# Optimization experiments

Hardware: AMD Instinct MI355X
Metric: run time of the kernel (lower is better)

## Reference

```python
import jax, jax.numpy as jnp
import numpy as np

B, S, HID = 4, 2048, 1024
NH, NKV, HD = 16, 4, 64
GROUPS = NH // NKV
SCALE = HD ** -0.5


def make_rope(seq_len, dim, base=10000.0):
    inv_freq = 1.0 / (base ** (np.arange(0, dim, 2, dtype=np.float32) / dim))
    t = np.arange(seq_len, dtype=np.float32)
    freqs = np.outer(t, inv_freq)                      # [S, D/2]
    emb = np.concatenate([freqs, freqs], axis=-1)      # [S, D] duplicated-half convention
    cos = jnp.asarray(np.cos(emb))[None, None]         # [1,1,S,D]
    sin = jnp.asarray(np.sin(emb))[None, None]
    return cos, sin


def setup_inputs() -> dict:
    key = jax.random.key(0)
    ks = jax.random.split(key, 8)
    hidden_states = jax.random.normal(ks[0], (B, S, HID), dtype=jnp.float32)
    cos, sin = make_rope(S, HD)
    std = HID ** -0.5
    Wq = jax.random.normal(ks[1], (NH * HD, HID), dtype=jnp.float32) * std
    bq = jnp.zeros((NH * HD,), dtype=jnp.float32)
    Wk = jax.random.normal(ks[2], (NKV * HD, HID), dtype=jnp.float32) * std
    bk = jnp.zeros((NKV * HD,), dtype=jnp.float32)
    Wv = jax.random.normal(ks[3], (NKV * HD, HID), dtype=jnp.float32) * std
    bv = jnp.zeros((NKV * HD,), dtype=jnp.float32)
    Wo = jax.random.normal(ks[4], (HID, NH * HD), dtype=jnp.float32) * std
    bo = jnp.zeros((HID,), dtype=jnp.float32)
    return dict(hidden_states=hidden_states, cos=cos, sin=sin,
                Wq=Wq, bq=bq, Wk=Wk, bk=bk, Wv=Wv, bv=bv, Wo=Wo, bo=bo)


def rotate_half(x):
    x1, x2 = jnp.split(x, 2, axis=-1)
    return jnp.concatenate([-x2, x1], axis=-1)


def reference(hidden_states, cos, sin, Wq, bq, Wk, bk, Wv, bv, Wo, bo):
    x = hidden_states  # [B,S,HID]
    q = (x @ Wq.T + bq).reshape(B, S, NH, HD).transpose(0, 2, 1, 3)    # [B,NH,S,D]
    k = (x @ Wk.T + bk).reshape(B, S, NKV, HD).transpose(0, 2, 1, 3)   # [B,NKV,S,D]
    v = (x @ Wv.T + bv).reshape(B, S, NKV, HD).transpose(0, 2, 1, 3)
    # RoPE
    q = q * cos + rotate_half(q) * sin
    k = k * cos + rotate_half(k) * sin
    # GQA: repeat_interleave kv heads to match q heads
    k = jnp.repeat(k, GROUPS, axis=1)  # [B,NH,S,D]
    v = jnp.repeat(v, GROUPS, axis=1)
    # scaled dot-product attention (no mask, no dropout at eval)
    scores = jnp.einsum('bhqd,bhkd->bhqk', q, k) * SCALE
    attn = jax.nn.softmax(scores, axis=-1)
    out = jnp.einsum('bhqk,bhkd->bhqd', attn, v)       # [B,NH,S,D]
    out = out.transpose(0, 2, 1, 3).reshape(B, S, NH * HD)
    return out @ Wo.T + bo
```

## Files before the change

### kernel.cpp

```cpp
#include <hip/hip_runtime.h>
#include <stdint.h>

#define S_LEN 2048
#define HIDDEN 1024
#define NHEADS 16
#define NKVH 4
#define HDIM 64

typedef __bf16 bf16x8 __attribute__((ext_vector_type(8)));
typedef __bf16 bf16x4 __attribute__((ext_vector_type(4)));
typedef float f32x4 __attribute__((ext_vector_type(4)));
typedef short s16x4 __attribute__((ext_vector_type(4)));
typedef unsigned short U16;

#define OFF_XB   0u
#define OFF_WQB  8388608u
#define OFF_WKB  9437184u
#define OFF_WVB  9699328u
#define OFF_WOB  9961472u
#define OFF_Q    11010048u
#define OFF_K    19398656u
#define OFF_V    21495808u
#define OFF_AWS  OFF_XB

static __device__ __forceinline__ U16 f2bf(float f){
    unsigned u;
    __builtin_memcpy(&u, &f, 4);
    u += 0x7FFFu + ((u >> 16) & 1u);
    return (U16)(u >> 16);
}
static __device__ __forceinline__ uint32_t pkbf(float lo, float hi){
    uint32_t a, b;
    __builtin_memcpy(&a, &lo, 4); a += 0x7FFFu + ((a >> 16) & 1u);
    __builtin_memcpy(&b, &hi, 4); b += 0x7FFFu + ((b >> 16) & 1u);
    return (a >> 16) | (b & 0xFFFF0000u);
}

typedef __attribute__((address_space(3))) uint32_t lds_u32;
typedef const __attribute__((address_space(1))) uint32_t glb_u32;
static __device__ __forceinline__ void glds16(const U16* g, U16* l){
    __builtin_amdgcn_global_load_lds((glb_u32*)g, (lds_u32*)l, 16, 0, 0);
}

__global__ void conv_kernel(const float* __restrict__ X,  const float* __restrict__ Wq,
                            const float* __restrict__ Wk, const float* __restrict__ Wv,
                            const float* __restrict__ Wo, U16* __restrict__ dst)
{
    size_t i4 = (size_t)blockIdx.x * 256 + threadIdx.x;
    size_t e = i4 * 4;
    const float* s;
    if (e < 8388608u)       s = X  + e;
    else if (e < 9437184u)  s = Wq + (e - 8388608u);
    else if (e < 9699328u)  s = Wk + (e - 9437184u);
    else if (e < 9961472u)  s = Wv + (e - 9699328u);
    else                    s = Wo + (e - 9961472u);
    float4 v = *(const float4*)s;
    uint2 o; o.x = pkbf(v.x, v.y); o.y = pkbf(v.z, v.w);
    *(uint2*)(dst + e) = o;
}

__global__ __launch_bounds__(256, 3)
void qkv_kernel(const U16* __restrict__ Xb,
                const U16* __restrict__ Wqb, const U16* __restrict__ Wkb, const U16* __restrict__ Wvb,
                const float* __restrict__ bq, const float* __restrict__ bk, const float* __restrict__ bv,
                const float* __restrict__ cosT, const float* __restrict__ sinT,
                U16* __restrict__ qws, U16* __restrict__ kws, U16* __restrict__ vtws)
{
    __shared__ __align__(16) U16 Asm[128 * 64];
    __shared__ __align__(16) U16 Bsm[128 * 64];

    const int mblk = blockIdx.x;
    const int nblk = blockIdx.y;
    const int tid  = threadIdx.x;
    const int wave = tid >> 6, lane = tid & 63;
    const int ln = lane & 15, quad = lane >> 4;
    const int wm = wave >> 1, wn = wave & 1;

    const U16* Wp; const float* biasp; int region;
    const int nbase = nblk * 128;
    if (nblk < 8)       { Wp = Wqb + (size_t)nbase * HIDDEN;          biasp = bq + nbase;          region = 0; }
    else if (nblk < 10) { Wp = Wkb + (size_t)(nbase - 1024) * HIDDEN; biasp = bk + (nbase - 1024); region = 1; }
    else                { Wp = Wvb + (size_t)(nbase - 1280) * HIDDEN; biasp = bv + (nbase - 1280); region = 2; }
    const U16* Xp = Xb + (size_t)mblk * 128 * HIDDEN;

    f32x4 acc[4][4];
    #pragma unroll
    for (int i = 0; i < 4; i++)
        #pragma unroll
        for (int j = 0; j < 4; j++) acc[i][j] = (f32x4){0.f, 0.f, 0.f, 0.f};

    const int l8 = lane >> 3;
    const int cg = (lane & 7) ^ l8;
    const int sw = ln & 7;

    for (int k0 = 0; k0 < HIDDEN; k0 += 64) {
        __syncthreads();
        #pragma unroll
        for (int t = 0; t < 4; t++) {
            int rbase = wave * 32 + t * 8;
            glds16(Xp + (size_t)(rbase + l8) * HIDDEN + k0 + cg * 8, &Asm[rbase * 64]);
            glds16(Wp + (size_t)(rbase + l8) * HIDDEN + k0 + cg * 8, &Bsm[rbase * 64]);
        }
        __syncthreads();

        bf16x8 af[4][2], bfr[4][2];
        #pragma unroll
        for (int i = 0; i < 4; i++)
            #pragma unroll
            for (int ks = 0; ks < 2; ks++) {
                af[i][ks]  = *(const bf16x8*)(&Asm[(wm * 64 + i * 16 + ln) * 64 + (((ks * 4 + quad) ^ sw) * 8)]);
                bfr[i][ks] = *(const bf16x8*)(&Bsm[(wn * 64 + i * 16 + ln) * 64 + (((ks * 4 + quad) ^ sw) * 8)]);
            }
        #pragma unroll
        for (int i = 0; i < 4; i++)
            #pragma unroll
            for (int j = 0; j < 4; j++) {
                acc[i][j] = __builtin_amdgcn_mfma_f32_16x16x32_bf16(af[i][0], bfr[j][0], acc[i][j], 0, 0, 0);
                acc[i][j] = __builtin_amdgcn_mfma_f32_16x16x32_bf16(af[i][1], bfr[j][1], acc[i][j], 0, 0, 0);
            }
    }

    float bias[4];
    #pragma unroll
    for (int j = 0; j < 4; j++) bias[j] = biasp[wn * 64 + j * 16 + ln];

    const float QSCALE = 0.125f * 1.44269504089f;

    if (region == 2) {
        #pragma unroll
        for (int i = 0; i < 4; i++) {
            int m0 = mblk * 128 + wm * 64 + i * 16 + quad * 4;
            int b = m0 >> 11;
            int st6 = m0 & (S_LEN - 1);
            int tile = st6 >> 6, soff = st6 & 63;
            #pragma unroll
            for (int j = 0; j < 4; j++) {
                int n2 = nbase - 1280 + wn * 64 + j * 16 + ln;
                int hh = n2 >> 6, d = n2 & 63;
                uint2 w;
                w.x = pkbf(acc[i][j][0] + bias[j], acc[i][j][1] + bias[j]);
                w.y = pkbf(acc[i][j][2] + bias[j], acc[i][j][3] + bias[j]);
                *(uint2*)(vtws + ((((size_t)b * NKVH + hh) * 32 + tile) * 64 + d) * 64 + soff) = w;
            }
        }
    } else {
        #pragma unroll
        for (int i = 0; i < 4; i++) {
            #pragma unroll
            for (int r = 0; r < 4; r++) {
                int m = mblk * 128 + wm * 64 + i * 16 + quad * 4 + r;
                int s = m & (S_LEN - 1), b = m >> 11;
                float vals[4];
                #pragma unroll
                for (int j = 0; j < 4; j++) vals[j] = acc[i][j][r] + bias[j];
                float outv[4];
                #pragma unroll
                for (int j = 0; j < 4; j++) {
                    int d = (wn * 64 + j * 16 + ln) & 63;
                    float c  = cosT[s * HDIM + d];
                    float sn = sinT[s * HDIM + d];
                    float partner = vals[j ^ 2];
                    float rot = (d < 32) ? -partner : partner;
                    outv[j] = vals[j] * c + rot * sn;
                }
                if (region == 0) {
                    #pragma unroll
                    for (int j = 0; j < 4; j++) {
                        int n = nbase + wn * 64 + j * 16 + ln;
                        int hh = n >> 6, d = n & 63;
                        qws[(((size_t)b * NHEADS + hh) * S_LEN + s) * HDIM + d] = f2bf(outv[j] * QSCALE);
                    }
                } else {
                    #pragma unroll
                    for (int j = 0; j < 4; j++) {
                        int n2 = nbase - 1024 + wn * 64 + j * 16 + ln;
                        int hh = n2 >> 6, d = n2 & 63;
                        kws[(((size_t)b * NKVH + hh) * S_LEN + s) * HDIM + d] = f2bf(outv[j]);
                    }
                }
            }
        }
    }
}

__global__ __launch_bounds__(256, 4)
void attn_kernel(const U16* __restrict__ qws, const U16* __restrict__ kws,
                 const U16* __restrict__ vtws, U16* __restrict__ aws)
{
    __shared__ __align__(16) U16 Ksm[2][64 * 64];
    __shared__ __align__(16) U16 VTsm[2][64 * 64];

    const int qt = blockIdx.x;
    const int hg = blockIdx.y;
    const int b = hg >> 4, h = hg & 15, hkv = h >> 2;
    const U16* Qh  = qws  + (size_t)hg * S_LEN * HDIM;
    const U16* Kh  = kws  + (size_t)(b * NKVH + hkv) * S_LEN * HDIM;
    const U16* VTh = vtws + (size_t)(b * NKVH + hkv) * HDIM * S_LEN;

    const int tid = threadIdx.x;
    const int wave = tid >> 6, lane = tid & 63;
    const int ln = lane & 15, quad = lane >> 4;
    const int sw = ln & 7;
    const int voff = (quad & 1) * 4;

    bf16x8 qf[2][2];
    #pragma unroll
    for (int i = 0; i < 2; i++)
        #pragma unroll
        for (int ks = 0; ks < 2; ks++) {
            int row = qt * 128 + wave * 32 + i * 16 + ln;
            qf[i][ks] = *(const bf16x8*)(Qh + (size_t)row * HDIM + ks * 32 + quad * 8);
        }

    float rsA[2] = {0.f, 0.f}, rsB[2] = {0.f, 0.f};
    f32x4 o_t[4][2];
    #pragma unroll
    for (int n = 0; n < 4; n++)
        #pragma unroll
        for (int i = 0; i < 2; i++) o_t[n][i] = (f32x4){0.f, 0.f, 0.f, 0.f};

    const int l8 = lane >> 3;
    const int cgk = (lane & 7) ^ l8;

    const int koff0 = ln * 64 + ((quad ^ sw) * 8);
    const int koff1 = ln * 64 + (((quad + 4) ^ sw) * 8);
    const int vbase = ln * 64 + voff;
    int cvo[4];
    #pragma unroll
    for (int j = 0; j < 4; j++) cvo[j] = (((j * 2 + (quad >> 1)) ^ sw) * 8);

    const U16* pk[2]; const U16* pv[2];
    U16* dK[2]; U16* dV[2];
    #pragma unroll
    for (int t = 0; t < 2; t++) {
        int c = wave * 2 + t;
        pk[t] = Kh  + (size_t)(c * 8 + l8) * HDIM + cgk * 8;
        pv[t] = VTh + (size_t)(c * 8 + l8) * 64  + cgk * 8;
        dK[t] = &Ksm[0][c * 8 * 64];
        dV[t] = &VTsm[0][c * 8 * 64];
    }

    #pragma unroll
    for (int t = 0; t < 2; t++) {
        glds16(pk[t], dK[t]);
        glds16(pv[t], dV[t]);
        pk[t] += 4096; pv[t] += 4096;
    }

    s16x4 pfp[2];
    pfp[0] = (s16x4){0, 0, 0, 0}; pfp[1] = (s16x4){0, 0, 0, 0};
    s16x4 vfp[4];
    #pragma unroll
    for (int n = 0; n < 4; n++) vfp[n] = (s16x4){0, 0, 0, 0};

    int p = 0;
    for (int kt = 0; kt < 32; kt++) {
        __syncthreads();

        if (kt < 31) {
            #pragma unroll
            for (int t = 0; t < 2; t++) {
                glds16(pk[t], dK[t] + (p ^ 1) * 4096);
                glds16(pv[t], dV[t] + (p ^ 1) * 4096);
                pk[t] += 4096; pv[t] += 4096;
            }
        }

        const U16* Kb = &Ksm[p][0];
        const U16* Vb = &VTsm[p][0];

        bf16x8 kfa = *(const bf16x8*)(Kb + koff0);
        bf16x8 kfb = *(const bf16x8*)(Kb + koff1);

        #pragma unroll
        for (int j = 0; j < 4; j++) {
            __builtin_amdgcn_s_setprio(1);
            f32x4 z[2];
            #pragma unroll
            for (int i = 0; i < 2; i++) {
                z[i] = (f32x4){0.f, 0.f, 0.f, 0.f};
                z[i] = __builtin_amdgcn_mfma_f32_16x16x32_bf16(kfa, qf[i][0], z[i], 0, 0, 0);
                z[i] = __builtin_amdgcn_mfma_f32_16x16x32_bf16(kfb, qf[i][1], z[i], 0, 0, 0);
            }
            #pragma unroll
            for (int n = 0; n < 4; n++)
                #pragma unroll
                for (int i = 0; i < 2; i++)
                    o_t[n][i] = __builtin_amdgcn_mfma_f32_16x16x16bf16_1k(vfp[n], pfp[i], o_t[n][i], 0, 0, 0);
            __builtin_amdgcn_s_setprio(0);

            if (j < 3) {
                kfa = *(const bf16x8*)(Kb + (j + 1) * 1024 + koff0);
                kfb = *(const bf16x8*)(Kb + (j + 1) * 1024 + koff1);
            }
            s16x4 vf[4];
            const U16* Vj = Vb + vbase + cvo[j];
            #pragma unroll
            for (int n = 0; n < 4; n++)
                vf[n] = *(const s16x4*)(Vj + n * 1024);
            __builtin_amdgcn_sched_barrier(0);

            s16x4 pf[2];
            #pragma unroll
            for (int i = 0; i < 2; i++) {
                bf16x4 pb;
                #pragma unroll
                for (int r = 0; r < 4; r++) {
                    float pe = __builtin_amdgcn_exp2f(z[i][r]);
                    if (r & 1) rsB[i] += pe; else rsA[i] += pe;
                    pb[r] = (__bf16)pe;
                }
                __builtin_memcpy(&pf[i], &pb, 8);
            }
            #pragma unroll
            for (int n = 0; n < 4; n++) vfp[n] = vf[n];
            pfp[0] = pf[0]; pfp[1] = pf[1];
        }
        p ^= 1;
    }

    #pragma unroll
    for (int n = 0; n < 4; n++)
        #pragma unroll
        for (int i = 0; i < 2; i++)
            o_t[n][i] = __builtin_amdgcn_mfma_f32_16x16x16bf16_1k(vfp[n], pfp[i], o_t[n][i], 0, 0, 0);

    float inv_li[2];
    #pragma unroll
    for (int i = 0; i < 2; i++) {
        float t = rsA[i] + rsB[i];
        t += __shfl_xor(t, 16);
        t += __shfl_xor(t, 32);
        inv_li[i] = 1.f / t;
    }
    #pragma unroll
    for (int n = 0; n < 4; n++)
        #pragma unroll
        for (int i = 0; i < 2; i++) {
            int q = qt * 128 + wave * 32 + i * 16 + ln;
            int d = n * 16 + quad * 4;
            uint2 w;
            w.x = pkbf(o_t[n][i][0] * inv_li[i], o_t[n][i][1] * inv_li[i]);
            w.y = pkbf(o_t[n][i][2] * inv_li[i], o_t[n][i][3] * inv_li[i]);
            *(uint2*)(aws + ((size_t)b * S_LEN + q) * (NHEADS * HDIM) + h * HDIM + d) = w;
        }
}

__global__ __launch_bounds__(256, 3)
void proj_kernel(const U16* __restrict__ A, const U16* __restrict__ Wob,
                 const float* __restrict__ bo, float* __restrict__ out)
{
    __shared__ __align__(16) U16 Asm[128 * 64];
    __shared__ __align__(16) U16 Bsm[128 * 64];

    const int mblk = blockIdx.x;
    const int nblk = blockIdx.y;
    const int tid  = threadIdx.x;
    const int wave = tid >> 6, lane = tid & 63;
    const int ln = lane & 15, quad = lane >> 4;
    const int wm = wave >> 1, wn = wave & 1;

    const int nbase = nblk * 128;
    const U16* Wp = Wob + (size_t)nbase * HIDDEN;
    const U16* Ap = A + (size_t)mblk * 128 * HIDDEN;

    f32x4 acc[4][4];
    #pragma unroll
    for (int i = 0; i < 4; i++)
        #pragma unroll
        for (int j = 0; j < 4; j++) acc[i][j] = (f32x4){0.f, 0.f, 0.f, 0.f};

    const int l8 = lane >> 3;
    const int cg = (lane & 7) ^ l8;
    const int sw = ln & 7;

    for (int k0 = 0; k0 < HIDDEN; k0 += 64) {
        __syncthreads();
        #pragma unroll
        for (int t = 0; t < 4; t++) {
            int rbase = wave * 32 + t * 8;
            glds16(Ap + (size_t)(rbase + l8) * HIDDEN + k0 + cg * 8, &Asm[rbase * 64]);
            glds16(Wp + (size_t)(rbase + l8) * HIDDEN + k0 + cg * 8, &Bsm[rbase * 64]);
        }
        __syncthreads();

        bf16x8 af[4][2], bfr[4][2];
        #pragma unroll
        for (int i = 0; i < 4; i++)
            #pragma unroll
            for (int ks = 0; ks < 2; ks++) {
                af[i][ks]  = *(const bf16x8*)(&Asm[(wm * 64 + i * 16 + ln) * 64 + (((ks * 4 + quad) ^ sw) * 8)]);
                bfr[i][ks] = *(const bf16x8*)(&Bsm[(wn * 64 + i * 16 + ln) * 64 + (((ks * 4 + quad) ^ sw) * 8)]);
            }
        #pragma unroll
        for (int i = 0; i < 4; i++)
            #pragma unroll
            for (int j = 0; j < 4; j++) {
                acc[i][j] = __builtin_amdgcn_mfma_f32_16x16x32_bf16(af[i][0], bfr[j][0], acc[i][j], 0, 0, 0);
                acc[i][j] = __builtin_amdgcn_mfma_f32_16x16x32_bf16(af[i][1], bfr[j][1], acc[i][j], 0, 0, 0);
            }
    }

    float bias[4];
    #pragma unroll
    for (int j = 0; j < 4; j++) bias[j] = bo[nbase + wn * 64 + j * 16 + ln];

    #pragma unroll
    for (int i = 0; i < 4; i++)
        #pragma unroll
        for (int r = 0; r < 4; r++) {
            int m = mblk * 128 + wm * 64 + i * 16 + quad * 4 + r;
            #pragma unroll
            for (int j = 0; j < 4; j++) {
                int n = nbase + wn * 64 + j * 16 + ln;
                out[(size_t)m * HIDDEN + n] = acc[i][j][r] + bias[j];
            }
        }
}

extern "C" void kernel_launch(void* const* d_in, const int* in_sizes, int n_in,
                              void* d_out, int out_size, void* d_ws, size_t ws_size,
                              hipStream_t stream)
{
    const float* X    = (const float*)d_in[0];
    const float* cosT = (const float*)d_in[1];
    const float* sinT = (const float*)d_in[2];
    const float* Wq   = (const float*)d_in[3];
    const float* bq   = (const float*)d_in[4];
    const float* Wk   = (const float*)d_in[5];
    const float* bk   = (const float*)d_in[6];
    const float* Wv   = (const float*)d_in[7];
    const float* bv   = (const float*)d_in[8];
    const float* Wo   = (const float*)d_in[9];
    const float* bo   = (const float*)d_in[10];
    float* out = (float*)d_out;

    U16* wsb = (U16*)d_ws;
    U16* Xb   = wsb + OFF_XB;
    U16* Wqb  = wsb + OFF_WQB;
    U16* Wkb  = wsb + OFF_WKB;
    U16* Wvb  = wsb + OFF_WVB;
    U16* Wob  = wsb + OFF_WOB;
    U16* qws  = wsb + OFF_Q;
    U16* kws  = wsb + OFF_K;
    U16* vtws = wsb + OFF_V;
    U16* aws  = wsb + OFF_AWS;

    conv_kernel<<<dim3(10752), 256, 0, stream>>>(X, Wq, Wk, Wv, Wo, wsb);
    qkv_kernel<<<dim3(64, 12), 256, 0, stream>>>(Xb, Wqb, Wkb, Wvb, bq, bk, bv, cosT, sinT, qws, kws, vtws);
    attn_kernel<<<dim3(16, 64), 256, 0, stream>>>(qws, kws, vtws, aws);
    proj_kernel<<<dim3(64, 8), 256, 0, stream>>>(aws, Wob, bo, out);
}
```

Before: 244.7 us.

## Use K=32 MFMA for PV product with permuted V-transpose layout

The PV product now uses 16x16x32 bf16 MFMAs in place of 16x16x16. Two 16-key score tiles are processed per step, so each P fragment packs eight probabilities. The projection kernel writes V-transposed with a permuted sequence offset so that each lane's 8-element V fragment lines up with the P element ordering. This halves the PV MFMA count and the number of LDS V reads, but raises register pressure from the doubled score and K fragments.

```diff
diff --git a/kernel.cpp b/kernel.cpp
--- a/kernel.cpp
+++ b/kernel.cpp
@@ -133,6 +133,7 @@
             int b = m0 >> 11;
             int st6 = m0 & (S_LEN - 1);
             int tile = st6 >> 6, soff = st6 & 63;
+            int sperm = (soff & 32) + (((soff & 15) >> 2) << 3) + (((soff >> 4) & 1) << 2);
             #pragma unroll
             for (int j = 0; j < 4; j++) {
                 int n2 = nbase - 1280 + wn * 64 + j * 16 + ln;
@@ -140,7 +141,7 @@
                 uint2 w;
                 w.x = pkbf(acc[i][j][0] + bias[j], acc[i][j][1] + bias[j]);
                 w.y = pkbf(acc[i][j][2] + bias[j], acc[i][j][3] + bias[j]);
-                *(uint2*)(vtws + ((((size_t)b * NKVH + hh) * 32 + tile) * 64 + d) * 64 + soff) = w;
+                *(uint2*)(vtws + ((((size_t)b * NKVH + hh) * 32 + tile) * 64 + d) * 64 + sperm) = w;
             }
         }
     } else {
@@ -201,7 +202,6 @@
     const int wave = tid >> 6, lane = tid & 63;
     const int ln = lane & 15, quad = lane >> 4;
     const int sw = ln & 7;
-    const int voff = (quad & 1) * 4;
 
     bf16x8 qf[2][2];
     #pragma unroll
@@ -224,10 +224,7 @@
 
     const int koff0 = ln * 64 + ((quad ^ sw) * 8);
     const int koff1 = ln * 64 + (((quad + 4) ^ sw) * 8);
-    const int vbase = ln * 64 + voff;
-    int cvo[4];
-    #pragma unroll
-    for (int j = 0; j < 4; j++) cvo[j] = (((j * 2 + (quad >> 1)) ^ sw) * 8);
+    const int vrow = ln * 64;
 
     const U16* pk[2]; const U16* pv[2];
     U16* dK[2]; U16* dV[2];
@@ -247,11 +244,12 @@
         pk[t] += 4096; pv[t] += 4096;
     }
 
-    s16x4 pfp[2];
-    pfp[0] = (s16x4){0, 0, 0, 0}; pfp[1] = (s16x4){0, 0, 0, 0};
-    s16x4 vfp[4];
-    #pragma unroll
-    for (int n = 0; n < 4; n++) vfp[n] = (s16x4){0, 0, 0, 0};
+    bf16x8 pfp[2];
+    #pragma unroll
+    for (int i = 0; i < 2; i++) pfp[i] = (bf16x8){0,0,0,0,0,0,0,0};
+    bf16x8 vfp[4];
+    #pragma unroll
+    for (int n = 0; n < 4; n++) vfp[n] = (bf16x8){0,0,0,0,0,0,0,0};
 
     int p = 0;
     for (int kt = 0; kt < 32; kt++) {
@@ -269,48 +267,56 @@
         const U16* Kb = &Ksm[p][0];
         const U16* Vb = &VTsm[p][0];
 
-        bf16x8 kfa = *(const bf16x8*)(Kb + koff0);
-        bf16x8 kfb = *(const bf16x8*)(Kb + koff1);
-
-        #pragma unroll
-        for (int j = 0; j < 4; j++) {
+        bf16x8 kf[2][2];
+        kf[0][0] = *(const bf16x8*)(Kb + koff0);
+        kf[0][1] = *(const bf16x8*)(Kb + koff1);
+        kf[1][0] = *(const bf16x8*)(Kb + 1024 + koff0);
+        kf[1][1] = *(const bf16x8*)(Kb + 1024 + koff1);
+
+        #pragma unroll
+        for (int pr = 0; pr < 2; pr++) {
             __builtin_amdgcn_s_setprio(1);
-            f32x4 z[2];
-            #pragma unroll
-            for (int i = 0; i < 2; i++) {
-                z[i] = (f32x4){0.f, 0.f, 0.f, 0.f};
-                z[i] = __builtin_amdgcn_mfma_f32_16x16x32_bf16(kfa, qf[i][0], z[i], 0, 0, 0);
-                z[i] = __builtin_amdgcn_mfma_f32_16x16x32_bf16(kfb, qf[i][1], z[i], 0, 0, 0);
-            }
+            f32x4 z[2][2];
+            #pragma unroll
+            for (int jj = 0; jj < 2; jj++)
+                #pragma unroll
+                for (int i = 0; i < 2; i++) {
+                    z[jj][i] = (f32x4){0.f, 0.f, 0.f, 0.f};
+                    z[jj][i] = __builtin_amdgcn_mfma_f32_16x16x32_bf16(kf[jj][0], qf[i][0], z[jj][i], 0, 0, 0);
+                    z[jj][i] = __builtin_amdgcn_mfma_f32_16x16x32_bf16(kf[jj][1], qf[i][1], z[jj][i], 0, 0, 0);
+                }
             #pragma unroll
             for (int n = 0; n < 4; n++)
                 #pragma unroll
                 for (int i = 0; i < 2; i++)
-                    o_t[n][i] = __builtin_amdgcn_mfma_f32_16x16x16bf16_1k(vfp[n], pfp[i], o_t[n][i], 0, 0, 0);
+                    o_t[n][i] = __builtin_amdgcn_mfma_f32_16x16x32_bf16(vfp[n], pfp[i], o_t[n][i], 0, 0, 0);
             __builtin_amdgcn_s_setprio(0);
 
-            if (j < 3) {
-                kfa = *(const bf16x8*)(Kb + (j + 1) * 1024 + koff0);
-                kfb = *(const bf16x8*)(Kb + (j + 1) * 1024 + koff1);
-            }
-            s16x4 vf[4];
-            const U16* Vj = Vb + vbase + cvo[j];
+            if (pr == 0) {
+                kf[0][0] = *(const bf16x8*)(Kb + 2048 + koff0);
+                kf[0][1] = *(const bf16x8*)(Kb + 2048 + koff1);
+                kf[1][0] = *(const bf16x8*)(Kb + 3072 + koff0);
+                kf[1][1] = *(const bf16x8*)(Kb + 3072 + koff1);
+            }
+            bf16x8 vf[4];
             #pragma unroll
             for (int n = 0; n < 4; n++)
-                vf[n] = *(const s16x4*)(Vj + n * 1024);
+                vf[n] = *(const bf16x8*)(Vb + n * 1024 + vrow + (((pr * 4 + quad) ^ sw) * 8));
             __builtin_amdgcn_sched_barrier(0);
 
-            s16x4 pf[2];
+            bf16x8 pf[2];
             #pragma unroll
             for (int i = 0; i < 2; i++) {
-                bf16x4 pb;
+                bf16x8 pb;
                 #pragma unroll
-                for (int r = 0; r < 4; r++) {
-                    float pe = __builtin_amdgcn_exp2f(z[i][r]);
-                    if (r & 1) rsB[i] += pe; else rsA[i] += pe;
-                    pb[r] = (__bf16)pe;
+                for (int e = 0; e < 4; e++) {
+                    float p0v = __builtin_amdgcn_exp2f(z[0][i][e]);
+                    float p1v = __builtin_amdgcn_exp2f(z[1][i][e]);
+                    if (e & 1) rsB[i] += p0v + p1v; else rsA[i] += p0v + p1v;
+                    pb[e]     = (__bf16)p0v;
+                    pb[e + 4] = (__bf16)p1v;
                 }
-                __builtin_memcpy(&pf[i], &pb, 8);
+                pf[i] = pb;
             }
             #pragma unroll
             for (int n = 0; n < 4; n++) vfp[n] = vf[n];
@@ -323,7 +329,7 @@
     for (int n = 0; n < 4; n++)
         #pragma unroll
         for (int i = 0; i < 2; i++)
-            o_t[n][i] = __builtin_amdgcn_mfma_f32_16x16x16bf16_1k(vfp[n], pfp[i], o_t[n][i], 0, 0, 0);
+            o_t[n][i] = __builtin_amdgcn_mfma_f32_16x16x32_bf16(vfp[n], pfp[i], o_t[n][i], 0, 0, 0);
 
     float inv_li[2];
     #pragma unroll
```

Measured after the change: 246.6 us. Within noise of the previous version (+0.8%).
